# Optimization experiments

Measured on AMD Instinct MI355X. Metric: run time of the kernel, lower is better.

The kernel has to match this reference:

```python
import jax, jax.numpy as jnp
import numpy as np

LSH_NUM_PROJS = 7
BLOCK_SIZE = 256
SAMPLE_SIZE = 256
B, H, N, D = 2, 16, 8192, 64


def _gray_perm(num_projs):
    # Gray-code ordering so adjacent hash buckets differ by 1 bit (AngularLSH.perm)
    a = np.array([0, 1], dtype=np.int32)
    for _ in range(num_projs - 1):
        a = np.concatenate([a, a[::-1] + a.shape[0]])
    return a

_PERM = jnp.asarray(_gray_perm(LSH_NUM_PROJS))
_ENC = 2 ** jnp.arange(LSH_NUM_PROJS, dtype=jnp.int32)


def lsh_hash(x, proj_dir):
    # x: [b,h,n,d], proj_dir: [1,1,d,r] -> bucket ids [b,h,n]
    proj = jnp.einsum('...nd,...dr->...nr', x, proj_dir)
    bits = (proj > 0).astype(jnp.int32)
    return _PERM[(bits * _ENC).sum(-1)]


def gather_seq(x, idx):
    # x: [b,h,n,d], idx: [b,h,s] -> [b,h,s,d]
    return jnp.take_along_axis(x, idx[..., None], axis=2)


def setup_inputs() -> dict:
    key = jax.random.key(0)
    kq, kk, kv, kp, ks = jax.random.split(key, 5)
    query = jax.random.normal(kq, (B, H, N, D), dtype=jnp.float32)
    key_t = jax.random.normal(kk, (B, H, N, D), dtype=jnp.float32)
    value = jax.random.normal(kv, (B, H, N, D), dtype=jnp.float32)
    proj_dir = jax.random.normal(kp, (1, 1, D, LSH_NUM_PROJS), dtype=jnp.float32)
    # uniform sampling WITHOUT replacement per (b,h), like torch.multinomial
    skeys = jax.random.split(ks, B * H)
    sampled_set = jax.vmap(lambda k: jax.random.permutation(k, N)[:SAMPLE_SIZE])(skeys)
    sampled_set = sampled_set.reshape(B, H, SAMPLE_SIZE).astype(jnp.int32)
    return {'query': query, 'key': key_t, 'value': value,
            'proj_dir': proj_dir, 'sampled_set': sampled_set}


def reference(query, key, value, proj_dir, sampled_set):
    b, h, n, d = query.shape
    scale = d ** -0.5
    neg_min = jnp.finfo(query.dtype).min

    # ---- 1. LSH-sort queries and keys (stable sort on bucket ids) ----
    q_idx = jnp.argsort(lsh_hash(query, proj_dir), axis=2, stable=True)
    k_idx = jnp.argsort(lsh_hash(key, proj_dir), axis=2, stable=True)
    q_idx_inv = jnp.argsort(q_idx, axis=2, stable=True)
    q_s = gather_seq(query, q_idx)
    k_s = gather_seq(key, k_idx)
    v_s = gather_seq(value, k_idx)

    # ---- 2. block-diagonal exact attention on sorted order ----
    nb = n // BLOCK_SIZE               # n divisible by block_size (8192/256=32)
    qbs = n // nb                       # query_block_size == 256 here
    qb = q_s.reshape(b, h, nb, qbs, d)
    kb = k_s.reshape(b, h, nb, BLOCK_SIZE, d)
    vb = v_s.reshape(b, h, nb, BLOCK_SIZE, d)
    qk = jnp.einsum('bhnqd,bhnkd->bhnqk', qb, kb) * scale
    lse_blk = jax.nn.logsumexp(qk, axis=-1, keepdims=True)
    attn_blk = jnp.einsum('bhnqk,bhnkd->bhnqd', jnp.exp(qk - lse_blk), vb)
    attn_blk = attn_blk.reshape(b, h, n, d)
    lse_blk = lse_blk.reshape(b, h, n, 1)

    # ---- 3. sampled-column residual attention ----
    k_sub = gather_seq(k_s, sampled_set)   # [b,h,S,d]
    v_sub = gather_seq(v_s, sampled_set)
    row_blk = (jnp.arange(n) // qbs)[None, None, :, None]            # [1,1,n,1]
    col_blk = (sampled_set // BLOCK_SIZE)[:, :, None, :]             # [b,h,1,S]
    in_block = row_blk == col_blk                                    # [b,h,n,S]
    sampled_cnt = SAMPLE_SIZE - in_block.sum(-1, keepdims=True).astype(query.dtype)
    bias = in_block.astype(query.dtype) * neg_min                    # mask double-counted cols
    qk_r = jnp.einsum('bhnd,bhsd->bhns', q_s, k_sub) * scale + bias
    lse_r = jax.nn.logsumexp(qk_r, axis=-1, keepdims=True)
    attn_r = jnp.einsum('bhns,bhsd->bhnd', jnp.exp(qk_r - lse_r), v_sub)
    # approximate_unsampled: rescale sampled mass to stand in for all
    # (n - block_size) out-of-block columns
    lse_r = lse_r + jnp.log((n - BLOCK_SIZE) / sampled_cnt)

    # ---- 4. combine the two attention estimates (add_self_attentions) ----
    lse = jnp.logaddexp(lse_blk, lse_r)
    c = jnp.exp(lse_blk - lse)
    attn = c * attn_blk + (1.0 - c) * attn_r

    # ---- 5. un-sort rows back to original query order ----
    attn = gather_seq(attn, q_idx_inv)
    return attn
```

## Files before the change

### kernel.cpp

```cpp
#include <hip/hip_runtime.h>
#include <math.h>

#define BH    32
#define NSEQ  8192
#define DDIM  64
#define NPROJ 7
#define BLK   256
#define NB    32
#define PITCH 72

typedef _Float16 v8h __attribute__((ext_vector_type(8)));
typedef float    v4f __attribute__((ext_vector_type(4)));

__global__ void hash_kernel(const float* __restrict__ query,
                            const float* __restrict__ key,
                            const float* __restrict__ proj,
                            int* __restrict__ buckets)
{
    const float* x = (blockIdx.y == 0) ? query : key;
    const int row0 = blockIdx.x * 64;
    const int t = threadIdx.x;

    __shared__ float tile[64][65];
    __shared__ float pd[64 * NPROJ];

    for (int i = t; i < 64 * NPROJ; i += 256) pd[i] = proj[i];

    const float4* src = (const float4*)(x + (size_t)row0 * DDIM);
    #pragma unroll
    for (int i = 0; i < 4; ++i) {
        int idx = t + i * 256;
        int r = idx >> 4, c4 = idx & 15;
        float4 v = src[r * 16 + c4];
        tile[r][c4 * 4 + 0] = v.x;
        tile[r][c4 * 4 + 1] = v.y;
        tile[r][c4 * 4 + 2] = v.z;
        tile[r][c4 * 4 + 3] = v.w;
    }
    __syncthreads();

    if (t < 64) {
        double acc[NPROJ];
        #pragma unroll
        for (int r = 0; r < NPROJ; ++r) acc[r] = 0.0;
        for (int d = 0; d < 64; ++d) {
            double xv = (double)tile[t][d];
            #pragma unroll
            for (int r = 0; r < NPROJ; ++r)
                acc[r] += xv * (double)pd[d * NPROJ + r];
        }
        int code = 0;
        #pragma unroll
        for (int r = 0; r < NPROJ; ++r)
            if (acc[r] > 0.0) code |= (1 << r);
        buckets[(size_t)blockIdx.y * (BH * NSEQ) + row0 + t] = code ^ (code >> 1);
    }
}

__global__ void sort_kernel(const int* __restrict__ buckets,
                            int* __restrict__ q_idx,
                            int* __restrict__ k_idx)
{
    const int bh = blockIdx.x;
    const int t = threadIdx.x;
    const int* b = buckets + (size_t)blockIdx.y * (BH * NSEQ) + (size_t)bh * NSEQ;
    int* out = ((blockIdx.y == 0) ? q_idx : k_idx) + (size_t)bh * NSEQ;

    __shared__ unsigned int cnt[128 * 64];
    __shared__ unsigned int rowsum[128];
    __shared__ unsigned int base[128];

    for (int v = 0; v < 128; ++v) cnt[v * 64 + t] = 0;
    __syncthreads();

    const int CH = NSEQ / 64;
    const int i0 = t * CH;
    for (int j = 0; j < CH; ++j) cnt[b[i0 + j] * 64 + t]++;
    __syncthreads();

    for (int v = t; v < 128; v += 64) {
        unsigned int s = 0;
        for (int tt = 0; tt < 64; ++tt) s += cnt[v * 64 + tt];
        rowsum[v] = s;
    }
    __syncthreads();

    if (t == 0) {
        unsigned int acc = 0;
        for (int v = 0; v < 128; ++v) { base[v] = acc; acc += rowsum[v]; }
    }
    __syncthreads();

    for (int v = t; v < 128; v += 64) {
        unsigned int acc = base[v];
        for (int tt = 0; tt < 64; ++tt) {
            unsigned int c = cnt[v * 64 + tt];
            cnt[v * 64 + tt] = acc;
            acc += c;
        }
    }
    __syncthreads();

    for (int j = 0; j < CH; ++j) {
        int v = b[i0 + j];
        out[cnt[v * 64 + t]++] = i0 + j;
    }
}

__global__ __launch_bounds__(256, 2) void attn_kernel(
        const float* __restrict__ query,
        const float* __restrict__ key,
        const float* __restrict__ value,
        const int* __restrict__ sampled,
        const int* __restrict__ q_idx,
        const int* __restrict__ k_idx,
        float* __restrict__ outp)
{
    const int qb = blockIdx.x;
    const int bh = blockIdx.y;
    const int t  = threadIdx.x;
    const int w    = t >> 6;
    const int lane = t & 63;
    const int quad = lane >> 4;
    const int nrow = lane & 15;

    __shared__ _Float16 Kc[64 * PITCH];
    __shared__ _Float16 Vt[64 * PITCH];
    __shared__ _Float16 Pb[4][64 * PITCH];
    __shared__ int   s_row[512];
    __shared__ float lb[512];
    __shared__ int   s_qi[256];
    __shared__ int   wb[4];

    const size_t bhN = (size_t)bh * NSEQ;

    {
        s_qi[t] = q_idx[bhN + qb * BLK + t];
        s_row[t] = k_idx[bhN + qb * BLK + t];
        int ss = sampled[bh * BLK + t];
        s_row[256 + t] = k_idx[bhN + ss];
        int sb = ss >> 8;
        unsigned long long mk = __ballot(sb == qb);
        if (lane == 0) wb[w] = __popcll(mk);
        __syncthreads();
        int cnt_in = wb[0] + wb[1] + wb[2] + wb[3];
        float J = __logf((float)(NSEQ - BLK) / (float)(BLK - cnt_in));
        lb[t] = -6.0f;
        lb[256 + t] = (sb == qb) ? -1.0e4f : (J - 6.0f);
    }

    v8h qf[4][2];
    #pragma unroll
    for (int mi = 0; mi < 4; ++mi) {
        int qi = q_idx[bhN + qb * BLK + w * 64 + mi * 16 + nrow];
        const float* qp = query + (bhN + (size_t)qi) * DDIM;
        #pragma unroll
        for (int kf = 0; kf < 2; ++kf) {
            const float4* q4 = (const float4*)(qp + kf * 32 + quad * 8);
            float4 x = q4[0], y = q4[1];
            v8h h;
            h[0]=(_Float16)x.x; h[1]=(_Float16)x.y; h[2]=(_Float16)x.z; h[3]=(_Float16)x.w;
            h[4]=(_Float16)y.x; h[5]=(_Float16)y.y; h[6]=(_Float16)y.z; h[7]=(_Float16)y.w;
            qf[mi][kf] = h;
        }
    }

    v4f Oacc[4][4];
    v4f lacc[4];
    #pragma unroll
    for (int mi = 0; mi < 4; ++mi) {
        lacc[mi] = (v4f){0.f, 0.f, 0.f, 0.f};
        #pragma unroll
        for (int di = 0; di < 4; ++di) Oacc[mi][di] = (v4f){0.f, 0.f, 0.f, 0.f};
    }
    const v8h ones = {(_Float16)1, (_Float16)1, (_Float16)1, (_Float16)1,
                      (_Float16)1, (_Float16)1, (_Float16)1, (_Float16)1};
    _Float16* Pw = Pb[w];

    for (int ch = 0; ch < 8; ++ch) {
        __syncthreads();
        {
            int r = t >> 2, seg = t & 3;
            int krow = s_row[ch * 64 + r];
            const float4* kp = (const float4*)(key + (bhN + (size_t)krow) * DDIM + seg * 16);
            float4 a0 = kp[0], a1 = kp[1], a2 = kp[2], a3 = kp[3];
            v8h h0, h1;
            h0[0]=(_Float16)a0.x; h0[1]=(_Float16)a0.y; h0[2]=(_Float16)a0.z; h0[3]=(_Float16)a0.w;
            h0[4]=(_Float16)a1.x; h0[5]=(_Float16)a1.y; h0[6]=(_Float16)a1.z; h0[7]=(_Float16)a1.w;
            h1[0]=(_Float16)a2.x; h1[1]=(_Float16)a2.y; h1[2]=(_Float16)a2.z; h1[3]=(_Float16)a2.w;
            h1[4]=(_Float16)a3.x; h1[5]=(_Float16)a3.y; h1[6]=(_Float16)a3.z; h1[7]=(_Float16)a3.w;
            *(v8h*)&Kc[r * PITCH + seg * 16] = h0;
            *(v8h*)&Kc[r * PITCH + seg * 16 + 8] = h1;
        }
        {
            int vk = t & 63, dg = t >> 6;
            int vrow = s_row[ch * 64 + vk];
            const float4* vp = (const float4*)(value + (bhN + (size_t)vrow) * DDIM + dg * 16);
            float4 b0 = vp[0], b1 = vp[1], b2 = vp[2], b3 = vp[3];
            float tmp[16] = {b0.x,b0.y,b0.z,b0.w, b1.x,b1.y,b1.z,b1.w,
                             b2.x,b2.y,b2.z,b2.w, b3.x,b3.y,b3.z,b3.w};
            #pragma unroll
            for (int i = 0; i < 16; ++i)
                Vt[(dg * 16 + i) * PITCH + vk] = (_Float16)tmp[i];
        }
        __syncthreads();

        float bb[4];
        #pragma unroll
        for (int ni = 0; ni < 4; ++ni) bb[ni] = lb[ch * 64 + ni * 16 + nrow];

        v8h kf[4][2], vb[4][2];
        #pragma unroll
        for (int ni = 0; ni < 4; ++ni)
            #pragma unroll
            for (int k2 = 0; k2 < 2; ++k2) {
                kf[ni][k2] = *(const v8h*)&Kc[(ni * 16 + nrow) * PITCH + k2 * 32 + quad * 8];
                vb[ni][k2] = *(const v8h*)&Vt[(ni * 16 + nrow) * PITCH + k2 * 32 + quad * 8];
            }

        #pragma unroll
        for (int mi = 0; mi < 4; ++mi) {
            v4f S[4];
            #pragma unroll
            for (int ni = 0; ni < 4; ++ni) {
                S[ni] = (v4f){0.f, 0.f, 0.f, 0.f};
                S[ni] = __builtin_amdgcn_mfma_f32_16x16x32_f16(qf[mi][0], kf[ni][0], S[ni], 0, 0, 0);
                S[ni] = __builtin_amdgcn_mfma_f32_16x16x32_f16(qf[mi][1], kf[ni][1], S[ni], 0, 0, 0);
            }
            #pragma unroll
            for (int ni = 0; ni < 4; ++ni) {
                #pragma unroll
                for (int r = 0; r < 4; ++r) {
                    float p = __expf(fmaf(S[ni][r], 0.125f, bb[ni]));
                    Pw[(mi * 16 + quad * 4 + r) * PITCH + ni * 16 + nrow] = (_Float16)p;
                }
            }
        }

        #pragma unroll
        for (int mi = 0; mi < 4; ++mi) {
            #pragma unroll
            for (int k2 = 0; k2 < 2; ++k2) {
                v8h pa = *(const v8h*)&Pw[(mi * 16 + nrow) * PITCH + k2 * 32 + quad * 8];
                lacc[mi] = __builtin_amdgcn_mfma_f32_16x16x32_f16(pa, ones, lacc[mi], 0, 0, 0);
                #pragma unroll
                for (int di = 0; di < 4; ++di)
                    Oacc[mi][di] = __builtin_amdgcn_mfma_f32_16x16x32_f16(pa, vb[di][k2], Oacc[mi][di], 0, 0, 0);
            }
        }
    }

    #pragma unroll
    for (int mi = 0; mi < 4; ++mi)
        #pragma unroll
        for (int r = 0; r < 4; ++r) {
            float inv = 1.0f / lacc[mi][r];
            #pragma unroll
            for (int di = 0; di < 4; ++di)
                Pw[(mi * 16 + quad * 4 + r) * PITCH + di * 16 + nrow] =
                    (_Float16)(Oacc[mi][di][r] * inv);
        }
    __syncthreads();

    #pragma unroll
    for (int p = 0; p < 4; ++p) {
        int row = p * 64 + (t >> 2);
        int seg = t & 3;
        const _Float16* src = &Pb[row >> 6][(row & 63) * PITCH + seg * 16];
        v8h x0 = *(const v8h*)src;
        v8h x1 = *(const v8h*)(src + 8);
        int qi = s_qi[row];
        float4* op = (float4*)(outp + (bhN + (size_t)qi) * DDIM + seg * 16);
        op[0] = make_float4((float)x0[0], (float)x0[1], (float)x0[2], (float)x0[3]);
        op[1] = make_float4((float)x0[4], (float)x0[5], (float)x0[6], (float)x0[7]);
        op[2] = make_float4((float)x1[0], (float)x1[1], (float)x1[2], (float)x1[3]);
        op[3] = make_float4((float)x1[4], (float)x1[5], (float)x1[6], (float)x1[7]);
    }
}

extern "C" void kernel_launch(void* const* d_in, const int* in_sizes, int n_in,
                              void* d_out, int out_size, void* d_ws, size_t ws_size,
                              hipStream_t stream) {
    (void)in_sizes; (void)n_in; (void)out_size; (void)ws_size;
    const float* query = (const float*)d_in[0];
    const float* key   = (const float*)d_in[1];
    const float* value = (const float*)d_in[2];
    const float* proj  = (const float*)d_in[3];
    const int* sampled = (const int*)d_in[4];
    float* out = (float*)d_out;

    int* buckets = (int*)d_ws;
    int* q_idx   = buckets + 2 * BH * NSEQ;
    int* k_idx   = q_idx + BH * NSEQ;

    hash_kernel<<<dim3(BH * NSEQ / 64, 2), 256, 0, stream>>>(query, key, proj, buckets);
    sort_kernel<<<dim3(BH, 2), 64, 0, stream>>>(buckets, q_idx, k_idx);
    attn_kernel<<<dim3(NB, BH), 256, 0, stream>>>(query, key, value, sampled,
                                                  q_idx, k_idx, out);
}
```

Before: 303.6 us.

## Parallelize hash and sort kernels, transpose attention MFMA layout, shrink LDS

The hash kernel now has all 256 threads each compute one row directly from global memory, instead of only 64 threads working from a shared tile. The sort kernel goes from 64 to 256 threads, using 16-bit counters, vectorized bucket loads and a shuffle-based prefix scan. The attention kernel swaps the MFMA operands so K is the A-operand. It uses exp2 with pre-scaled biases, stages P in a smaller per-wave buffer processed in two 32-column halves, and aliases the output staging buffer onto the K/V region. Lower LDS use allows occupancy 3, at the cost of more register pressure and more complex indexing.

Measured after the change: 299.6 us. Within noise of the previous version (-1.3%).

```diff
diff --git a/kernel.cpp b/kernel.cpp
--- a/kernel.cpp
+++ b/kernel.cpp
@@ -8,106 +8,135 @@
 #define BLK   256
 #define NB    32
 #define PITCH 72
+#define PPITCH 40
+#define LOG2E 1.44269504f
+#define SC2   0.180336881f
 
 typedef _Float16 v8h __attribute__((ext_vector_type(8)));
+typedef _Float16 v4h __attribute__((ext_vector_type(4)));
 typedef float    v4f __attribute__((ext_vector_type(4)));
 
-__global__ void hash_kernel(const float* __restrict__ query,
-                            const float* __restrict__ key,
-                            const float* __restrict__ proj,
-                            int* __restrict__ buckets)
+__global__ __launch_bounds__(256) void hash_kernel(
+        const float* __restrict__ query,
+        const float* __restrict__ key,
+        const float* __restrict__ proj,
+        int* __restrict__ buckets)
 {
     const float* x = (blockIdx.y == 0) ? query : key;
-    const int row0 = blockIdx.x * 64;
     const int t = threadIdx.x;
-
-    __shared__ float tile[64][65];
-    __shared__ float pd[64 * NPROJ];
-
-    for (int i = t; i < 64 * NPROJ; i += 256) pd[i] = proj[i];
-
-    const float4* src = (const float4*)(x + (size_t)row0 * DDIM);
-    #pragma unroll
-    for (int i = 0; i < 4; ++i) {
-        int idx = t + i * 256;
-        int r = idx >> 4, c4 = idx & 15;
-        float4 v = src[r * 16 + c4];
-        tile[r][c4 * 4 + 0] = v.x;
-        tile[r][c4 * 4 + 1] = v.y;
-        tile[r][c4 * 4 + 2] = v.z;
-        tile[r][c4 * 4 + 3] = v.w;
-    }
-    __syncthreads();
-
-    if (t < 64) {
-        double acc[NPROJ];
-        #pragma unroll
-        for (int r = 0; r < NPROJ; ++r) acc[r] = 0.0;
-        for (int d = 0; d < 64; ++d) {
-            double xv = (double)tile[t][d];
+    const int row = blockIdx.x * 256 + t;
+
+    __shared__ double pdd[64 * NPROJ];
+    for (int i = t; i < 64 * NPROJ; i += 256) pdd[i] = (double)proj[i];
+    __syncthreads();
+
+    const float4* rp = (const float4*)(x + (size_t)row * DDIM);
+    double acc[NPROJ];
+    #pragma unroll
+    for (int r = 0; r < NPROJ; ++r) acc[r] = 0.0;
+
+    #pragma unroll
+    for (int i = 0; i < 16; ++i) {
+        float4 v = rp[i];
+        float e[4] = {v.x, v.y, v.z, v.w};
+        #pragma unroll
+        for (int c = 0; c < 4; ++c) {
+            double xv = (double)e[c];
+            const int d = i * 4 + c;
             #pragma unroll
             for (int r = 0; r < NPROJ; ++r)
-                acc[r] += xv * (double)pd[d * NPROJ + r];
-        }
-        int code = 0;
-        #pragma unroll
-        for (int r = 0; r < NPROJ; ++r)
-            if (acc[r] > 0.0) code |= (1 << r);
-        buckets[(size_t)blockIdx.y * (BH * NSEQ) + row0 + t] = code ^ (code >> 1);
-    }
+                acc[r] += xv * pdd[d * NPROJ + r];
+        }
+    }
+    int code = 0;
+    #pragma unroll
+    for (int r = 0; r < NPROJ; ++r)
+        if (acc[r] > 0.0) code |= (1 << r);
+    buckets[(size_t)blockIdx.y * (BH * NSEQ) + row] = code ^ (code >> 1);
 }
 
-__global__ void sort_kernel(const int* __restrict__ buckets,
-                            int* __restrict__ q_idx,
-                            int* __restrict__ k_idx)
+#define SCNT 258
+__global__ __launch_bounds__(256) void sort_kernel(
+        const int* __restrict__ buckets,
+        int* __restrict__ q_idx,
+        int* __restrict__ k_idx)
 {
     const int bh = blockIdx.x;
     const int t = threadIdx.x;
+    const int lane = t & 63, w = t >> 6;
     const int* b = buckets + (size_t)blockIdx.y * (BH * NSEQ) + (size_t)bh * NSEQ;
     int* out = ((blockIdx.y == 0) ? q_idx : k_idx) + (size_t)bh * NSEQ;
 
-    __shared__ unsigned int cnt[128 * 64];
-    __shared__ unsigned int rowsum[128];
-    __shared__ unsigned int base[128];
-
-    for (int v = 0; v < 128; ++v) cnt[v * 64 + t] = 0;
-    __syncthreads();
-
-    const int CH = NSEQ / 64;
-    const int i0 = t * CH;
-    for (int j = 0; j < CH; ++j) cnt[b[i0 + j] * 64 + t]++;
-    __syncthreads();
-
-    for (int v = t; v < 128; v += 64) {
+    __shared__ unsigned short cnt[128 * SCNT];
+    __shared__ unsigned int partial[256];
+    __shared__ unsigned int wsum[4];
+
+    unsigned int* cz = (unsigned int*)cnt;
+    for (int i = t; i < 128 * SCNT / 2; i += 256) cz[i] = 0;
+
+    int4 rv[8];
+    const int4* b4 = (const int4*)b;
+    #pragma unroll
+    for (int s = 0; s < 8; ++s) rv[s] = b4[t * 8 + s];
+    __syncthreads();
+
+    #pragma unroll
+    for (int s = 0; s < 8; ++s) {
+        cnt[rv[s].x * SCNT + t]++;
+        cnt[rv[s].y * SCNT + t]++;
+        cnt[rv[s].z * SCNT + t]++;
+        cnt[rv[s].w * SCNT + t]++;
+    }
+    __syncthreads();
+
+    const int v0 = t >> 1, tt0 = (t & 1) * 128;
+    {
         unsigned int s = 0;
-        for (int tt = 0; tt < 64; ++tt) s += cnt[v * 64 + tt];
-        rowsum[v] = s;
-    }
-    __syncthreads();
-
-    if (t == 0) {
-        unsigned int acc = 0;
-        for (int v = 0; v < 128; ++v) { base[v] = acc; acc += rowsum[v]; }
-    }
-    __syncthreads();
-
-    for (int v = t; v < 128; v += 64) {
-        unsigned int acc = base[v];
-        for (int tt = 0; tt < 64; ++tt) {
-            unsigned int c = cnt[v * 64 + tt];
-            cnt[v * 64 + tt] = acc;
-            acc += c;
-        }
-    }
-    __syncthreads();
-
-    for (int j = 0; j < CH; ++j) {
-        int v = b[i0 + j];
-        out[cnt[v * 64 + t]++] = i0 + j;
+        for (int j = 0; j < 128; ++j) s += cnt[v0 * SCNT + tt0 + j];
+        partial[t] = s;
+    }
+    __syncthreads();
+
+    unsigned int chunkoff;
+    {
+        unsigned int x = partial[t], own = x;
+        #pragma unroll
+        for (int d = 1; d < 64; d <<= 1) {
+            unsigned int y = __shfl_up(x, d);
+            if (lane >= d) x += y;
+        }
+        if (lane == 63) wsum[w] = x;
+        __syncthreads();
+        unsigned int wb0 = 0;
+        if (w == 1) wb0 = wsum[0];
+        else if (w == 2) wb0 = wsum[0] + wsum[1];
+        else if (w == 3) wb0 = wsum[0] + wsum[1] + wsum[2];
+        chunkoff = x - own + wb0;
+    }
+
+    {
+        unsigned int s = chunkoff;
+        for (int j = 0; j < 128; ++j) {
+            unsigned short c = cnt[v0 * SCNT + tt0 + j];
+            cnt[v0 * SCNT + tt0 + j] = (unsigned short)s;
+            s += c;
+        }
+    }
+    __syncthreads();
+
+    const int i0 = t * 32;
+    #pragma unroll
+    for (int s = 0; s < 8; ++s) {
+        int4 q = rv[s];
+        int j4 = i0 + s * 4;
+        { unsigned short p = cnt[q.x * SCNT + t]++; out[p] = j4 + 0; }
+        { unsigned short p = cnt[q.y * SCNT + t]++; out[p] = j4 + 1; }
+        { unsigned short p = cnt[q.z * SCNT + t]++; out[p] = j4 + 2; }
+        { unsigned short p = cnt[q.w * SCNT + t]++; out[p] = j4 + 3; }
     }
 }
 
-__global__ __launch_bounds__(256, 2) void attn_kernel(
+__global__ __launch_bounds__(256, 3) void attn_kernel(
         const float* __restrict__ query,
         const float* __restrict__ key,
         const float* __restrict__ value,
@@ -124,13 +153,15 @@
     const int quad = lane >> 4;
     const int nrow = lane & 15;
 
-    __shared__ _Float16 Kc[64 * PITCH];
-    __shared__ _Float16 Vt[64 * PITCH];
-    __shared__ _Float16 Pb[4][64 * PITCH];
-    __shared__ int   s_row[512];
-    __shared__ float lb[512];
-    __shared__ int   s_qi[256];
-    __shared__ int   wb[4];
+    __shared__ __align__(16) unsigned char smem[38912];
+    _Float16* Kc = (_Float16*)smem;
+    _Float16* Vt = (_Float16*)(smem + 9216);
+    _Float16* Pb = (_Float16*)(smem + 18432);
+    _Float16* Ob = (_Float16*)smem;
+    __shared__ int s_row[512];
+    __shared__ __align__(16) float lb[512];
+    __shared__ int s_qi[256];
+    __shared__ int wb[4];
 
     const size_t bhN = (size_t)bh * NSEQ;
 
@@ -145,44 +176,44 @@
         __syncthreads();
         int cnt_in = wb[0] + wb[1] + wb[2] + wb[3];
         float J = __logf((float)(NSEQ - BLK) / (float)(BLK - cnt_in));
-        lb[t] = -6.0f;
-        lb[256 + t] = (sb == qb) ? -1.0e4f : (J - 6.0f);
+        lb[t] = -6.0f * LOG2E;
+        lb[256 + t] = (sb == qb) ? -3.0e4f : (J - 6.0f) * LOG2E;
     }
 
     v8h qf[4][2];
     #pragma unroll
-    for (int mi = 0; mi < 4; ++mi) {
-        int qi = q_idx[bhN + qb * BLK + w * 64 + mi * 16 + nrow];
+    for (int ni = 0; ni < 4; ++ni) {
+        int qi = s_qi[w * 64 + ni * 16 + nrow];
         const float* qp = query + (bhN + (size_t)qi) * DDIM;
         #pragma unroll
-        for (int kf = 0; kf < 2; ++kf) {
-            const float4* q4 = (const float4*)(qp + kf * 32 + quad * 8);
-            float4 x = q4[0], y = q4[1];
+        for (int k2 = 0; k2 < 2; ++k2) {
+            const float4* q4 = (const float4*)(qp + k2 * 32 + quad * 8);
+            float4 a = q4[0], bvec = q4[1];
             v8h h;
-            h[0]=(_Float16)x.x; h[1]=(_Float16)x.y; h[2]=(_Float16)x.z; h[3]=(_Float16)x.w;
-            h[4]=(_Float16)y.x; h[5]=(_Float16)y.y; h[6]=(_Float16)y.z; h[7]=(_Float16)y.w;
-            qf[mi][kf] = h;
+            h[0]=(_Float16)a.x; h[1]=(_Float16)a.y; h[2]=(_Float16)a.z; h[3]=(_Float16)a.w;
+            h[4]=(_Float16)bvec.x; h[5]=(_Float16)bvec.y; h[6]=(_Float16)bvec.z; h[7]=(_Float16)bvec.w;
+            qf[ni][k2] = h;
         }
     }
 
     v4f Oacc[4][4];
     v4f lacc[4];
     #pragma unroll
-    for (int mi = 0; mi < 4; ++mi) {
-        lacc[mi] = (v4f){0.f, 0.f, 0.f, 0.f};
-        #pragma unroll
-        for (int di = 0; di < 4; ++di) Oacc[mi][di] = (v4f){0.f, 0.f, 0.f, 0.f};
+    for (int ni = 0; ni < 4; ++ni) {
+        lacc[ni] = (v4f){0.f, 0.f, 0.f, 0.f};
+        #pragma unroll
+        for (int mi2 = 0; mi2 < 4; ++mi2) Oacc[mi2][ni] = (v4f){0.f, 0.f, 0.f, 0.f};
     }
     const v8h ones = {(_Float16)1, (_Float16)1, (_Float16)1, (_Float16)1,
                       (_Float16)1, (_Float16)1, (_Float16)1, (_Float16)1};
-    _Float16* Pw = Pb[w];
+    _Float16* Pw = Pb + w * 64 * PPITCH;
 
     for (int ch = 0; ch < 8; ++ch) {
         __syncthreads();
         {
             int r = t >> 2, seg = t & 3;
-            int krow = s_row[ch * 64 + r];
-            const float4* kp = (const float4*)(key + (bhN + (size_t)krow) * DDIM + seg * 16);
+            int kr = s_row[ch * 64 + r];
+            const float4* kp = (const float4*)(key + (bhN + (size_t)kr) * DDIM + seg * 16);
             float4 a0 = kp[0], a1 = kp[1], a2 = kp[2], a3 = kp[3];
             v8h h0, h1;
             h0[0]=(_Float16)a0.x; h0[1]=(_Float16)a0.y; h0[2]=(_Float16)a0.z; h0[3]=(_Float16)a0.w;
@@ -193,80 +224,80 @@
             *(v8h*)&Kc[r * PITCH + seg * 16 + 8] = h1;
         }
         {
-            int vk = t & 63, dg = t >> 6;
-            int vrow = s_row[ch * 64 + vk];
-            const float4* vp = (const float4*)(value + (bhN + (size_t)vrow) * DDIM + dg * 16);
-            float4 b0 = vp[0], b1 = vp[1], b2 = vp[2], b3 = vp[3];
-            float tmp[16] = {b0.x,b0.y,b0.z,b0.w, b1.x,b1.y,b1.z,b1.w,
-                             b2.x,b2.y,b2.z,b2.w, b3.x,b3.y,b3.z,b3.w};
-            #pragma unroll
-            for (int i = 0; i < 16; ++i)
-                Vt[(dg * 16 + i) * PITCH + vk] = (_Float16)tmp[i];
+            int kq = t & 15, dg = t >> 4;
+            float la[4][4];
+            #pragma unroll
+            for (int c = 0; c < 4; ++c) {
+                int vr = s_row[ch * 64 + kq * 4 + c];
+                float4 v = *(const float4*)(value + (bhN + (size_t)vr) * DDIM + dg * 4);
+                la[c][0] = v.x; la[c][1] = v.y; la[c][2] = v.z; la[c][3] = v.w;
+            }
+            #pragma unroll
+            for (int dd = 0; dd < 4; ++dd) {
+                v4h h;
+                h[0]=(_Float16)la[0][dd]; h[1]=(_Float16)la[1][dd];
+                h[2]=(_Float16)la[2][dd]; h[3]=(_Float16)la[3][dd];
+                *(v4h*)&Vt[(dg * 4 + dd) * PITCH + kq * 4] = h;
+            }
         }
         __syncthreads();
 
-        float bb[4];
-        #pragma unroll
-        for (int ni = 0; ni < 4; ++ni) bb[ni] = lb[ch * 64 + ni * 16 + nrow];
-
-        v8h kf[4][2], vb[4][2];
-        #pragma unroll
-        for (int ni = 0; ni < 4; ++ni)
-            #pragma unroll
-            for (int k2 = 0; k2 < 2; ++k2) {
-                kf[ni][k2] = *(const v8h*)&Kc[(ni * 16 + nrow) * PITCH + k2 * 32 + quad * 8];
-                vb[ni][k2] = *(const v8h*)&Vt[(ni * 16 + nrow) * PITCH + k2 * 32 + quad * 8];
-            }
-
-        #pragma unroll
-        for (int mi = 0; mi < 4; ++mi) {
-            v4f S[4];
+        #pragma unroll
+        for (int ks = 0; ks < 2; ++ks) {
+            #pragma unroll
+            for (int mi = 0; mi < 2; ++mi) {
+                v4f bb = *(const v4f*)&lb[ch * 64 + ks * 32 + mi * 16 + quad * 4];
+                const int krow = ks * 32 + mi * 16 + nrow;
+                v8h ka0 = *(const v8h*)&Kc[krow * PITCH + quad * 8];
+                v8h ka1 = *(const v8h*)&Kc[krow * PITCH + 32 + quad * 8];
+                #pragma unroll
+                for (int ni = 0; ni < 4; ++ni) {
+                    v4f S = (v4f){0.f, 0.f, 0.f, 0.f};
+                    S = __builtin_amdgcn_mfma_f32_16x16x32_f16(ka0, qf[ni][0], S, 0, 0, 0);
+                    S = __builtin_amdgcn_mfma_f32_16x16x32_f16(ka1, qf[ni][1], S, 0, 0, 0);
+                    v4h ph;
+                    #pragma unroll
+                    for (int r = 0; r < 4; ++r)
+                        ph[r] = (_Float16)__builtin_amdgcn_exp2f(fmaf(S[r], SC2, bb[r]));
+                    *(v4h*)&Pw[(ni * 16 + nrow) * PPITCH + mi * 16 + quad * 4] = ph;
+                }
+            }
+            v8h pbv[4];
             #pragma unroll
             for (int ni = 0; ni < 4; ++ni) {
-                S[ni] = (v4f){0.f, 0.f, 0.f, 0.f};
-                S[ni] = __builtin_amdgcn_mfma_f32_16x16x32_f16(qf[mi][0], kf[ni][0], S[ni], 0, 0, 0);
-                S[ni] = __builtin_amdgcn_mfma_f32_16x16x32_f16(qf[mi][1], kf[ni][1], S[ni], 0, 0, 0);
-            }
-            #pragma unroll
-            for (int ni = 0; ni < 4; ++ni) {
+                pbv[ni] = *(const v8h*)&Pw[(ni * 16 + nrow) * PPITCH + quad * 8];
+                lacc[ni] = __builtin_amdgcn_mfma_f32_16x16x32_f16(ones, pbv[ni], lacc[ni], 0, 0, 0);
+            }
+            #pragma unroll
+            for (int mi2 = 0; mi2 < 4; ++mi2) {
+                v8h va = *(const v8h*)&Vt[(mi2 * 16 + nrow) * PITCH + ks * 32 + quad * 8];
                 #pragma unroll
-                for (int r = 0; r < 4; ++r) {
-                    float p = __expf(fmaf(S[ni][r], 0.125f, bb[ni]));
-                    Pw[(mi * 16 + quad * 4 + r) * PITCH + ni * 16 + nrow] = (_Float16)p;
-                }
-            }
-        }
-
-        #pragma unroll
-        for (int mi = 0; mi < 4; ++mi) {
-            #pragma unroll
-            for (int k2 = 0; k2 < 2; ++k2) {
-                v8h pa = *(const v8h*)&Pw[(mi * 16 + nrow) * PITCH + k2 * 32 + quad * 8];
-                lacc[mi] = __builtin_amdgcn_mfma_f32_16x16x32_f16(pa, ones, lacc[mi], 0, 0, 0);
-                #pragma unroll
-                for (int di = 0; di < 4; ++di)
-                    Oacc[mi][di] = __builtin_amdgcn_mfma_f32_16x16x32_f16(pa, vb[di][k2], Oacc[mi][di], 0, 0, 0);
-            }
-        }
-    }
-
-    #pragma unroll
-    for (int mi = 0; mi < 4; ++mi)
-        #pragma unroll
-        for (int r = 0; r < 4; ++r) {
-            float inv = 1.0f / lacc[mi][r];
-            #pragma unroll
-            for (int di = 0; di < 4; ++di)
-                Pw[(mi * 16 + quad * 4 + r) * PITCH + di * 16 + nrow] =
-                    (_Float16)(Oacc[mi][di][r] * inv);
-        }
+                for (int ni = 0; ni < 4; ++ni)
+                    Oacc[mi2][ni] = __builtin_amdgcn_mfma_f32_16x16x32_f16(va, pbv[ni], Oacc[mi2][ni], 0, 0, 0);
+            }
+        }
+    }
+
+    __syncthreads();
+    #pragma unroll
+    for (int ni = 0; ni < 4; ++ni) {
+        float inv = 1.0f / lacc[ni][0];
+        #pragma unroll
+        for (int mi2 = 0; mi2 < 4; ++mi2) {
+            v4h h;
+            #pragma unroll
+            for (int r = 0; r < 4; ++r)
+                h[r] = (_Float16)(Oacc[mi2][ni][r] * inv);
+            *(v4h*)&Ob[(w * 64 + ni * 16 + nrow) * PITCH + mi2 * 16 + quad * 4] = h;
+        }
+    }
     __syncthreads();
 
     #pragma unroll
     for (int p = 0; p < 4; ++p) {
         int row = p * 64 + (t >> 2);
         int seg = t & 3;
-        const _Float16* src = &Pb[row >> 6][(row & 63) * PITCH + seg * 16];
+        const _Float16* src = &Ob[row * PITCH + seg * 16];
         v8h x0 = *(const v8h*)src;
         v8h x1 = *(const v8h*)(src + 8);
         int qi = s_qi[row];
@@ -293,8 +324,8 @@
     int* q_idx   = buckets + 2 * BH * NSEQ;
     int* k_idx   = q_idx + BH * NSEQ;
 
-    hash_kernel<<<dim3(BH * NSEQ / 64, 2), 256, 0, stream>>>(query, key, proj, buckets);
-    sort_kernel<<<dim3(BH, 2), 64, 0, stream>>>(buckets, q_idx, k_idx);
+    hash_kernel<<<dim3(BH * NSEQ / 256, 2), 256, 0, stream>>>(query, key, proj, buckets);
+    sort_kernel<<<dim3(BH, 2), 256, 0, stream>>>(buckets, q_idx, k_idx);
     attn_kernel<<<dim3(NB, BH), 256, 0, stream>>>(query, key, value, sampled,
                                                   q_idx, k_idx, out);
 }
```
